# Kernel optimization log

Measured on AMD Instinct MI355X. Metric: run time of the kernel, lower is better.

## Reference

```python
import jax, jax.numpy as jnp
import numpy as np
from jax import lax

BATCH, C, HH, WW = 4, 3, 512, 512


def _dark_min(x, patch):
    # min over channels, reflect-pad, min over patch x patch window (torch unfold+min)
    pad = (patch - 1) // 2
    m = jnp.min(x, axis=1, keepdims=True)                      # [B,1,H,W]
    m = jnp.pad(m, ((0, 0), (0, 0), (pad, pad), (pad, pad)), mode='reflect')
    return lax.reduce_window(m, jnp.array(jnp.inf, m.dtype), lax.min,
                             (1, 1, patch, patch), (1, 1, 1, 1), 'VALID')


def _soft_thresh(x, lam):
    return jnp.sign(x) * jnp.maximum(jnp.abs(x) - lam, 0.0)


def _conv3x3(x, w):
    return lax.conv_general_dilated(x, w, (1, 1), 'SAME',
                                    dimension_numbers=('NCHW', 'OIHW', 'NCHW'))


def setup_inputs() -> dict:
    key = jax.random.key(0)
    names = ['I', 't_p', 'B_p', 'B', 't', 'J', 'G', 'H', 'P', 'Q', 'u', 'v', 'X', 'Y']
    keys = jax.random.split(key, len(names) + 2)
    inp = {n: jax.random.uniform(keys[i], (BATCH, C, HH, WW), dtype=jnp.float32)
           for i, n in enumerate(names)}
    for g in ['gamma_1', 'gamma_2', 'gamma_3', 'gamma_4', 'gamma_5']:
        inp[g] = jnp.array([3.001], dtype=jnp.float32)
    inp['t1d_w'] = jax.random.normal(keys[-2], (1, 3, 1, 1), dtype=jnp.float32) * 0.3
    inp['hnet_w'] = jax.random.normal(keys[-1], (3, 3, 3, 3), dtype=jnp.float32) * 0.1
    inp['patch_size'] = 35
    return inp


def _forward(I, t_p, B_p, B, t, J, G, H, P, Q, u, v, X, Y,
             gamma_1, gamma_2, gamma_3, gamma_4, gamma_5, t1d_w, hnet_w, patch_size):
    lam1, lam2, lam3, lam4, lam5 = 1.0, 0.7, 0.3, 1.0, 1.0

    # ---- get_mean_value + mapping_index (vectorized over batch) ----
    mean = jnp.mean(J, axis=(2, 3))                 # [B,3]
    idx = jnp.argsort(mean, axis=1)                 # ascending, like torch.sort
    ms = jnp.take_along_axis(mean, idx, axis=1)     # sorted means
    gather = lambda k: jnp.take_along_axis(J, idx[:, k][:, None, None, None], axis=1)
    J_l, J_m, J_s = gather(2), gather(1), gather(0)           # [B,1,H,W]
    bar = lambda k: ms[:, k][:, None, None, None]
    J_m = J_m + (bar(2) - bar(1)) * J_l
    J_s = J_s + (bar(2) - bar(0)) * J_l
    ch = jnp.arange(3)[None, :]                     # scatter channels back
    J = jnp.where((ch == idx[:, 1:2])[:, :, None, None], J_m, J)
    J = jnp.where((ch == idx[:, 0:1])[:, :, None, None], J_s, J)

    # ---- B update (spatial mean broadcast back) ----
    Bn = (lam3 * B_p - lam1 * (J * t - I) * (1.0 - t)) / (lam1 * (1.0 - t) ** 2 + lam3)
    Bn = jnp.mean(Bn, axis=(2, 3), keepdims=True) * jnp.ones_like(I)

    # ---- t update + 1x1 conv + channel replicate ----
    tn = (lam2 * t_p + gamma_4 * H - lam1 * (Bn - I) * (J - Bn) - X) / \
         (lam1 * (J - Bn) ** 2 + lam2 + gamma_4)
    t1 = jnp.einsum('oc,bchw->bohw', t1d_w[:, :, 0, 0], tn)   # [B,1,H,W]
    tn = jnp.concatenate([t1, t1, t1], axis=1)

    # ---- J, u, v updates ----
    Jn = (lam1 * (tn * (I - Bn * (1.0 - tn))) + gamma_3 * G + gamma_4 * u
          - gamma_5 * v - Y + gamma_5) / (lam1 * tn * tn + gamma_3 + gamma_4 + gamma_5)
    un = (gamma_1 * u + gamma_4 * Jn) / (gamma_1 + gamma_4)
    vn = (gamma_2 * v - gamma_5 * Jn + gamma_5) / (gamma_2 + gamma_5)

    # ---- H_Net (conv stand-in for RDN), dual updates ----
    Hn = _conv3x3(tn + X / gamma_4, hnet_w)
    Xn = X + gamma_4 * (tn - Hn)
    Yn = Y + gamma_3 * (Jn - G)

    # ---- dark channel + soft threshold ----
    M_u = _dark_min(un, patch_size)
    M_v = _dark_min(vn, patch_size)
    Pn = _soft_thresh(M_u, lam4 / gamma_1)
    Qn = _soft_thresh(M_v, lam5 / gamma_1)

    return (Bn, tn, Jn, G, Hn, Pn, Qn, un, vn, Xn, Yn, gamma_3)


def reference(I, t_p, B_p, B, t, J, G, H, P, Q, u, v, X, Y,
              gamma_1, gamma_2, gamma_3, gamma_4, gamma_5, t1d_w, hnet_w, patch_size):
    return _forward(I, t_p, B_p, B, t, J, G, H, P, Q, u, v, X, Y,
                    gamma_1, gamma_2, gamma_3, gamma_4, gamma_5, t1d_w, hnet_w, patch_size)
```

## Files before the change

kernel.cpp:

```cpp
#include <hip/hip_runtime.h>
#include <math.h>

#define W_ 512
#define H_ 512
#define HW_ 262144
#define HW4_ 65536
#define CHW_ 786432

#define O_Bn 0
#define O_tn 3145728
#define O_Jn 6291456
#define O_G  9437184
#define O_Hn 12582912
#define O_Pn 15728640
#define O_Qn 16777216
#define O_un 17825792
#define O_vn 20971520
#define O_Xn 24117248
#define O_Yn 27262976
#define O_g3 30408704

#define LAM2 0.7f
#define LAM3 0.3f

#define WS_SUMS   0
#define WS_ALPHA  8192
#define WS_IDX2   8204
#define WS_BNS    8208
#define WS_SCR    16384

typedef float nfloat4 __attribute__((ext_vector_type(4)));

__device__ __forceinline__ void nt_store4(float4 v, float4* p) {
    nfloat4 nv; nv.x = v.x; nv.y = v.y; nv.z = v.z; nv.w = v.w;
    __builtin_nontemporal_store(nv, (nfloat4*)p);
}

__global__ __launch_bounds__(256) void kRed(const float* __restrict__ J,
                                            const float* __restrict__ tt,
                                            const float* __restrict__ B_p,
                                            const float* __restrict__ I,
                                            float* __restrict__ sums) {
    int blk = blockIdx.x;
    int b = blk >> 7, chunk = blk & 127;
    size_t pb = (size_t)b * (CHW_ / 4);
    size_t cb = (size_t)chunk * 512;
    const float4* J4 = (const float4*)J;
    const float4* t4 = (const float4*)tt;
    const float4* B4 = (const float4*)B_p;
    const float4* I4 = (const float4*)I;

    float aJ[3] = {0.f, 0.f, 0.f};
    float a1[3] = {0.f, 0.f, 0.f};
    float a2[9] = {0.f, 0.f, 0.f, 0.f, 0.f, 0.f, 0.f, 0.f, 0.f};

    #pragma unroll
    for (int k = 0; k < 2; ++k) {
        size_t o = cb + threadIdx.x + k * 256;
        float4 j0 = J4[pb + 0 * HW4_ + o];
        float4 j1 = J4[pb + 1 * HW4_ + o];
        float4 j2 = J4[pb + 2 * HW4_ + o];
        #pragma unroll
        for (int c = 0; c < 3; ++c) {
            float4 tv = t4[pb + (size_t)c * HW4_ + o];
            float4 bp = B4[pb + (size_t)c * HW4_ + o];
            float4 iv = I4[pb + (size_t)c * HW4_ + o];
            float4 jc = (c == 0) ? j0 : (c == 1 ? j1 : j2);
#define REDC(m) { \
            float omt = 1.f - tv.m; \
            float r = 1.f / (omt * omt + LAM3); \
            float g = tv.m * omt * r; \
            aJ[c] += jc.m; \
            a1[c] += (LAM3 * bp.m - (jc.m * tv.m - iv.m) * omt) * r; \
            a2[0 * 3 + c] += j0.m * g; \
            a2[1 * 3 + c] += j1.m * g; \
            a2[2 * 3 + c] += j2.m * g; }
            REDC(x) REDC(y) REDC(z) REDC(w)
#undef REDC
        }
    }

    float vals[15];
    #pragma unroll
    for (int c = 0; c < 3; ++c) { vals[c] = aJ[c]; vals[3 + c] = a1[c]; }
    #pragma unroll
    for (int s = 0; s < 9; ++s) vals[6 + s] = a2[s];

    __shared__ float lds[4][15];
    int lane = threadIdx.x & 63, w = threadIdx.x >> 6;
    #pragma unroll
    for (int s = 0; s < 15; ++s) {
        float v = vals[s];
        #pragma unroll
        for (int off = 32; off; off >>= 1) v += __shfl_down(v, off, 64);
        if (lane == 0) lds[w][s] = v;
    }
    __syncthreads();
    if (threadIdx.x < 15) {
        int s = threadIdx.x;
        sums[blk * 16 + s] = lds[0][s] + lds[1][s] + lds[2][s] + lds[3][s];
    }
}

__global__ __launch_bounds__(256) void kFin(const float* __restrict__ sums,
                     float* __restrict__ alpha, int* __restrict__ idx2,
                     float* __restrict__ BnS,
                     const float* __restrict__ g3p, float* __restrict__ outg3) {
    __shared__ float part[64][4];
    __shared__ float tot[4][15];
    int t = threadIdx.x;
    int g = t >> 2, sub = t & 3;
    if (g < 60) {
        int b = g / 15, s = g % 15;
        const float* p = sums + (size_t)b * 128 * 16 + s;
        float acc = 0.f;
        #pragma unroll 8
        for (int ch = sub; ch < 128; ch += 4) acc += p[ch * 16];
        part[g][sub] = acc;
    }
    __syncthreads();
    if (t < 60) {
        tot[t / 15][t % 15] = (part[t][0] + part[t][1]) + (part[t][2] + part[t][3]);
    }
    __syncthreads();
    if (t < 4) {
        const float invHW = 1.0f / (float)HW_;
        float m[3] = {tot[t][0] * invHW, tot[t][1] * invHW, tot[t][2] * invHW};
        int r[3];
        #pragma unroll
        for (int i = 0; i < 3; ++i) {
            int ri = 0;
            #pragma unroll
            for (int j = 0; j < 3; ++j)
                if (j != i && (m[j] < m[i] || (m[j] == m[i] && j < i))) ri++;
            r[i] = ri;
        }
        int idx[3]; float ms[3];
        #pragma unroll
        for (int i = 0; i < 3; ++i) { idx[r[i]] = i; ms[r[i]] = m[i]; }
        idx2[t] = idx[2];
        float a[3] = {0.f, 0.f, 0.f};
        a[idx[1]] = ms[2] - ms[1];
        a[idx[0]] = ms[2] - ms[0];
        #pragma unroll
        for (int c = 0; c < 3; ++c) {
            alpha[t * 3 + c] = a[c];
            BnS[t * 3 + c] = (tot[t][3 + c] - a[c] * tot[t][6 + idx[2] * 3 + c]) * invHW;
        }
    }
    if (t == 0) *outg3 = g3p[0];
}

__global__ __launch_bounds__(256) void kMain(
    const float* __restrict__ I, const float* __restrict__ t_p,
    const float* __restrict__ Hm, const float* __restrict__ Xm,
    const float* __restrict__ J, const float* __restrict__ u,
    const float* __restrict__ v, const float* __restrict__ Y,
    const float* __restrict__ G,
    const float* __restrict__ g1p, const float* __restrict__ g2p,
    const float* __restrict__ g3p, const float* __restrict__ g4p,
    const float* __restrict__ g5p, const float* __restrict__ t1w,
    const float* __restrict__ alpha, const int* __restrict__ idx2,
    const float* __restrict__ BnS,
    float* __restrict__ out, float* __restrict__ scr)
{
    __shared__ float pad[2][2][560];

    int id = blockIdx.x * 256 + threadIdx.x;
    int b = id >> 16, q = id & (HW4_ - 1);
    float g1 = g1p[0], g2 = g2p[0], g3 = g3p[0], g4 = g4p[0], g5 = g5p[0];
    float wc[3] = {t1w[0], t1w[1], t1w[2]};
    int i2 = idx2[b];
    size_t pb = (size_t)b * (CHW_ / 4);
    const float4* I4p = (const float4*)I;
    const float4* tp4p = (const float4*)t_p;
    const float4* H4p = (const float4*)Hm;
    const float4* X4p = (const float4*)Xm;
    const float4* J4p = (const float4*)J;
    const float4* u4p = (const float4*)u;
    const float4* v4p = (const float4*)v;
    const float4* Y4p = (const float4*)Y;
    const float4* G4p = (const float4*)G;
    float4* o4 = (float4*)out;

    float4 Jl = J4p[pb + (size_t)i2 * HW4_ + q];
    float4 t1 = make_float4(0.f, 0.f, 0.f, 0.f);
    float4 Isv[3]; float Bsv[3];
    const float den2 = LAM2 + g4;
    #pragma unroll
    for (int c = 0; c < 3; ++c) {
        size_t o = pb + (size_t)c * HW4_ + q;
        float4 I4 = I4p[o], tp4 = tp4p[o], H4 = H4p[o], X4 = X4p[o], Jv = J4p[o];
        float al = alpha[b * 3 + c], Bnv = BnS[b * 3 + c];
        float wcc = wc[c];
#define STEP1(m) { \
        float d_ = (Jv.m + al * Jl.m) - Bnv; \
        float tnr_ = (LAM2 * tp4.m + g4 * H4.m - (Bnv - I4.m) * d_ - X4.m) / (d_ * d_ + den2); \
        t1.m += wcc * tnr_; }
        STEP1(x) STEP1(y) STEP1(z) STEP1(w)
#undef STEP1
        Isv[c] = I4; Bsv[c] = Bnv;
    }
    float g345 = g3 + g4 + g5;
    float4 invDen;
    invDen.x = 1.f / (t1.x * t1.x + g345);
    invDen.y = 1.f / (t1.y * t1.y + g345);
    invDen.z = 1.f / (t1.z * t1.z + g345);
    invDen.w = 1.f / (t1.w * t1.w + g345);
    float invDu = 1.f / (g1 + g4), invDv = 1.f / (g2 + g5);
    float4 cu = make_float4(1e30f, 1e30f, 1e30f, 1e30f);
    float4 cv = cu;
    #pragma unroll
    for (int c = 0; c < 3; ++c) {
        size_t o = pb + (size_t)c * HW4_ + q;
        float4 u4 = u4p[o], v4 = v4p[o], Y4 = Y4p[o], G4 = G4p[o];
        float Bnv = Bsv[c];
        float4 Jn4, un4, vn4, Yn4;
#define STEP2(m) { \
        float Jn_ = (t1.m * (Isv[c].m - Bnv * (1.f - t1.m)) + g3 * G4.m + g4 * u4.m \
                     - g5 * v4.m - Y4.m + g5) * invDen.m; \
        float un_ = (g1 * u4.m + g4 * Jn_) * invDu; \
        float vn_ = (g2 * v4.m - g5 * Jn_ + g5) * invDv; \
        Jn4.m = Jn_; un4.m = un_; vn4.m = vn_; \
        Yn4.m = Y4.m + g3 * (Jn_ - G4.m); \
        cu.m = fminf(cu.m, un_); cv.m = fminf(cv.m, vn_); }
        STEP2(x) STEP2(y) STEP2(z) STEP2(w)
#undef STEP2
        nt_store4(make_float4(Bnv, Bnv, Bnv, Bnv), &o4[O_Bn / 4 + o]);
        o4[O_tn / 4 + o] = t1;
        nt_store4(Jn4, &o4[O_Jn / 4 + o]);
        nt_store4(G4,  &o4[O_G  / 4 + o]);
        nt_store4(un4, &o4[O_un / 4 + o]);
        nt_store4(vn4, &o4[O_vn / 4 + o]);
        nt_store4(Yn4, &o4[O_Yn / 4 + o]);
    }

    int t = threadIdx.x;
    int rrow = t >> 7;
    int x0 = (t & 127) * 4;
    pad[0][rrow][17 + x0 + 0] = cu.x;
    pad[0][rrow][17 + x0 + 1] = cu.y;
    pad[0][rrow][17 + x0 + 2] = cu.z;
    pad[0][rrow][17 + x0 + 3] = cu.w;
    pad[1][rrow][17 + x0 + 0] = cv.x;
    pad[1][rrow][17 + x0 + 1] = cv.y;
    pad[1][rrow][17 + x0 + 2] = cv.z;
    pad[1][rrow][17 + x0 + 3] = cv.w;
    __syncthreads();
    if (t < 136) {
        int which = t / 34, e = t % 34;
        int tens = which >> 1, rw = which & 1;
        int j   = (e < 17) ? e : (529 + (e - 17));
        int src = (e < 17) ? (34 - j) : (1056 - j);
        pad[tens][rw][j] = pad[tens][rw][src];
    }
    __syncthreads();

    int y0b = (blockIdx.x & 255) * 2;
    int yg = y0b + rrow;
    #pragma unroll
    for (int tens = 0; tens < 2; ++tens) {
        const float* rowp = &pad[tens][rrow][0];
        const float4* rp4 = (const float4*)(rowp + x0);
        float4 qv = rp4[0];
        float a0 = qv.x, a1 = qv.y, a2 = qv.z;
        float mc = qv.w;
        #pragma unroll
        for (int i = 1; i < 8; ++i) {
            qv = rp4[i];
            mc = fminf(mc, fminf(fminf(qv.x, qv.y), fminf(qv.z, qv.w)));
        }
        qv = rp4[8];
        mc = fminf(mc, fminf(qv.x, fminf(qv.y, qv.z)));
        float a35 = qv.w;
        qv = rp4[9];
        float a36 = qv.x, a37 = qv.y;
        float4 r;
        r.x = fminf(fminf(a0, a1), fminf(a2, mc));
        r.y = fminf(fminf(a1, a2), fminf(mc, a35));
        r.z = fminf(fminf(a2, mc), fminf(a35, a36));
        r.w = fminf(fminf(mc, a35), fminf(a36, a37));
        *(float4*)(scr + (size_t)(tens * 4 + b) * HW_ + yg * W_ + x0) = r;
    }
}

__global__ __launch_bounds__(256) void kTail(const float* __restrict__ scr,
                                             const float* __restrict__ hw,
                                             const float* __restrict__ g1p,
                                             const float* __restrict__ g4p,
                                             float* __restrict__ out) {
    __shared__ float A_lds[3][4][528];
    __shared__ float wsh[81];
    int t = threadIdx.x;

    if (blockIdx.x < 2048) {
        int tensor = blockIdx.x >> 10;
        int lid = ((blockIdx.x & 1023) << 8) + t;
        int b = lid >> 16, qq = lid & (HW4_ - 1);
        int y = qq >> 7, xq = (qq & 127) << 2;
        const float* R = scr + (size_t)(tensor * 4 + b) * HW_;
        float4 m = make_float4(1e30f, 1e30f, 1e30f, 1e30f);
        #pragma unroll
        for (int k = 0; k < 35; ++k) {
            int yy = y + k - 17;
            yy = yy < 0 ? -yy : (yy >= H_ ? 2 * H_ - 2 - yy : yy);
            float4 r4 = *(const float4*)(R + yy * W_ + xq);
            m.x = fminf(m.x, r4.x); m.y = fminf(m.y, r4.y);
            m.z = fminf(m.z, r4.z); m.w = fminf(m.w, r4.w);
        }
        float lam = 1.0f / g1p[0];
        float4 r;
#define SOFT(m_, r_) { float s = (m_ > 0.f) ? 1.f : (m_ < 0.f ? -1.f : 0.f); \
                       r_ = s * fmaxf(fabsf(m_) - lam, 0.f); }
        SOFT(m.x, r.x) SOFT(m.y, r.y) SOFT(m.z, r.z) SOFT(m.w, r.w)
#undef SOFT
        nt_store4(r, (float4*)(out + (tensor ? O_Qn : O_Pn) + b * HW_ + y * W_ + xq));
    } else {
        int cblk = blockIdx.x - 2048;
        int b = cblk >> 8;
        int y0 = (cblk & 255) * 2;
        float g4 = g4p[0], ig4 = 1.f / g4;
        const float* tn0 = out + O_tn + (size_t)b * CHW_;
        const float* Xb  = out + O_Xn;
        (void)Xb;
        if (t < 81) wsh[t] = hw[t];
        #pragma unroll
        for (int k = 0; k < 6; ++k) {
            int g = t + 256 * k;
            int i = g >> 9, r = (g >> 7) & 3, xq = (g & 127) << 2;
            int yy = y0 - 1 + r;
            float4 A4;
            if (yy >= 0 && yy < H_) {
                const float* Xrow =  nullptr;
                (void)Xrow;
                A4 = make_float4(0.f, 0.f, 0.f, 0.f);
            }
            (void)A4; (void)i; (void)r; (void)xq; (void)yy;
        }
    }
}

__global__ __launch_bounds__(256) void kTail2(const float* __restrict__ scr,
                                              const float* __restrict__ Xm,
                                              const float* __restrict__ hw,
                                              const float* __restrict__ g1p,
                                              const float* __restrict__ g4p,
                                              float* __restrict__ out) {
    __shared__ float A_lds[3][4][528];
    __shared__ float wsh[81];
    int t = threadIdx.x;

    if (blockIdx.x < 2048) {
        int tensor = blockIdx.x >> 10;
        int lid = ((blockIdx.x & 1023) << 8) + t;
        int b = lid >> 16, qq = lid & (HW4_ - 1);
        int y = qq >> 7, xq = (qq & 127) << 2;
        const float* R = scr + (size_t)(tensor * 4 + b) * HW_;
        float4 m = make_float4(1e30f, 1e30f, 1e30f, 1e30f);
        #pragma unroll
        for (int k = 0; k < 35; ++k) {
            int yy = y + k - 17;
            yy = yy < 0 ? -yy : (yy >= H_ ? 2 * H_ - 2 - yy : yy);
            float4 r4 = *(const float4*)(R + yy * W_ + xq);
            m.x = fminf(m.x, r4.x); m.y = fminf(m.y, r4.y);
            m.z = fminf(m.z, r4.z); m.w = fminf(m.w, r4.w);
        }
        float lam = 1.0f / g1p[0];
        float4 r;
#define SOFT(m_, r_) { float s = (m_ > 0.f) ? 1.f : (m_ < 0.f ? -1.f : 0.f); \
                       r_ = s * fmaxf(fabsf(m_) - lam, 0.f); }
        SOFT(m.x, r.x) SOFT(m.y, r.y) SOFT(m.z, r.z) SOFT(m.w, r.w)
#undef SOFT
        nt_store4(r, (float4*)(out + (tensor ? O_Qn : O_Pn) + b * HW_ + y * W_ + xq));
    } else {
        int cblk = blockIdx.x - 2048;
        int b = cblk >> 8;
        int y0 = (cblk & 255) * 2;
        float g4 = g4p[0], ig4 = 1.f / g4;
        const float* tn0 = out + O_tn + (size_t)b * CHW_;
        if (t < 81) wsh[t] = hw[t];
        #pragma unroll
        for (int k = 0; k < 6; ++k) {
            int g = t + 256 * k;
            int i = g >> 9, r = (g >> 7) & 3, xq = (g & 127) << 2;
            int yy = y0 - 1 + r;
            float4 A4 = make_float4(0.f, 0.f, 0.f, 0.f);
            if (yy >= 0 && yy < H_) {
                float4 tn4 = *(const float4*)(tn0 + yy * W_ + xq);
                float4 X4  = *(const float4*)(Xm + (size_t)(b * 3 + i) * HW_ + yy * W_ + xq);
                A4.x = tn4.x + X4.x * ig4; A4.y = tn4.y + X4.y * ig4;
                A4.z = tn4.z + X4.z * ig4; A4.w = tn4.w + X4.w * ig4;
            }
            *(float4*)(&A_lds[i][r][4 + xq]) = A4;
        }
        if (t < 24) {
            int pair = t >> 1, side = t & 1;
            A_lds[pair >> 2][pair & 3][side ? 516 : 3] = 0.f;
        }
        __syncthreads();

        int tl = t & 127, r_out = t >> 7;
        float acc[3][4] = {{0.f,0.f,0.f,0.f},{0.f,0.f,0.f,0.f},{0.f,0.f,0.f,0.f}};
        #pragma unroll
        for (int i = 0; i < 3; ++i) {
            #pragma unroll
            for (int ky = 0; ky < 3; ++ky) {
                const float* Ar = &A_lds[i][r_out + ky][0];
                const float* wp0 = &wsh[0 * 27 + i * 9 + ky * 3];
                const float* wp1 = &wsh[1 * 27 + i * 9 + ky * 3];
                const float* wp2 = &wsh[2 * 27 + i * 9 + ky * 3];
                float w00 = wp0[0], w01 = wp0[1], w02 = wp0[2];
                float w10 = wp1[0], w11 = wp1[1], w12 = wp1[2];
                float w20 = wp2[0], w21 = wp2[1], w22 = wp2[2];
                #pragma unroll
                for (int j = 0; j < 4; ++j) {
                    int x = tl + 128 * j;
                    float am = Ar[3 + x], a0 = Ar[4 + x], ap = Ar[5 + x];
                    acc[0][j] += w00 * am + w01 * a0 + w02 * ap;
                    acc[1][j] += w10 * am + w11 * a0 + w12 * ap;
                    acc[2][j] += w20 * am + w21 * a0 + w22 * ap;
                }
            }
        }
        int yg = y0 + r_out;
        #pragma unroll
        for (int o = 0; o < 3; ++o) {
            #pragma unroll
            for (int j = 0; j < 4; ++j) {
                int x = tl + 128 * j;
                size_t oo = (size_t)(b * 3 + o) * HW_ + yg * W_ + x;
                float hn = acc[o][j];
                float Ac = A_lds[o][r_out + 1][4 + x];
                __builtin_nontemporal_store(hn, &out[O_Hn + oo]);
                __builtin_nontemporal_store(g4 * (Ac - hn), &out[O_Xn + oo]);
            }
        }
    }
}

extern "C" void kernel_launch(void* const* d_in, const int* in_sizes, int n_in,
                              void* d_out, int out_size, void* d_ws, size_t ws_size,
                              hipStream_t stream) {
    (void)in_sizes; (void)n_in; (void)out_size; (void)ws_size;
    const float* I   = (const float*)d_in[0];
    const float* t_p = (const float*)d_in[1];
    const float* B_p = (const float*)d_in[2];
    const float* tt  = (const float*)d_in[4];
    const float* J   = (const float*)d_in[5];
    const float* G   = (const float*)d_in[6];
    const float* Hm  = (const float*)d_in[7];
    const float* u   = (const float*)d_in[10];
    const float* v   = (const float*)d_in[11];
    const float* X   = (const float*)d_in[12];
    const float* Y   = (const float*)d_in[13];
    const float* g1  = (const float*)d_in[14];
    const float* g2  = (const float*)d_in[15];
    const float* g3  = (const float*)d_in[16];
    const float* g4  = (const float*)d_in[17];
    const float* g5  = (const float*)d_in[18];
    const float* t1w = (const float*)d_in[19];
    const float* hw  = (const float*)d_in[20];
    float* out = (float*)d_out;
    float* ws  = (float*)d_ws;

    float* sums  = ws + WS_SUMS;
    float* alpha = ws + WS_ALPHA;
    int*   idx2  = (int*)(ws + WS_IDX2);
    float* BnS   = ws + WS_BNS;
    float* scr   = ws + WS_SCR;

    kRed<<<512, 256, 0, stream>>>(J, tt, B_p, I, sums);
    kFin<<<1, 256, 0, stream>>>(sums, alpha, idx2, BnS, g3, out + O_g3);
    kMain<<<1024, 256, 0, stream>>>(I, t_p, Hm, X, J, u, v, Y, G,
                                    g1, g2, g3, g4, g5, t1w, alpha, idx2, BnS,
                                    out, scr);
    kTail2<<<3072, 256, 0, stream>>>(scr, X, hw, g1, g4, out);
}
```

Before: 310.6 us.

## Fuse conv stage into main kernel and replace finalize kernel with atomics

The single-block finalize kernel is removed: kRed now atomically accumulates per-batch sums into a zeroed workspace, and each kMain block recomputes sort/alpha/BnS from those sums in one thread. The 3x3 conv (Hn, Xn) moves into kMain, which builds its LDS input tile from registers plus recomputed halo rows, so tn is no longer re-read from global memory. The tail kernel keeps only the vertical min and soft threshold. The cost is recomputing t1 for halo rows, a memset launch, atomic order nondeterminism, and more LDS and registers in kMain.

```diff
diff --git a/kernel.cpp b/kernel.cpp
--- a/kernel.cpp
+++ b/kernel.cpp
@@ -23,10 +23,7 @@
 #define LAM2 0.7f
 #define LAM3 0.3f
 
-#define WS_SUMS   0
-#define WS_ALPHA  8192
-#define WS_IDX2   8204
-#define WS_BNS    8208
+#define WS_ACC    0
 #define WS_SCR    16384
 
 typedef float nfloat4 __attribute__((ext_vector_type(4)));
@@ -40,7 +37,7 @@
                                             const float* __restrict__ tt,
                                             const float* __restrict__ B_p,
                                             const float* __restrict__ I,
-                                            float* __restrict__ sums) {
+                                            float* __restrict__ acc) {
     int blk = blockIdx.x;
     int b = blk >> 7, chunk = blk & 127;
     size_t pb = (size_t)b * (CHW_ / 4);
@@ -98,57 +95,9 @@
     __syncthreads();
     if (threadIdx.x < 15) {
         int s = threadIdx.x;
-        sums[blk * 16 + s] = lds[0][s] + lds[1][s] + lds[2][s] + lds[3][s];
-    }
-}
-
-__global__ __launch_bounds__(256) void kFin(const float* __restrict__ sums,
-                     float* __restrict__ alpha, int* __restrict__ idx2,
-                     float* __restrict__ BnS,
-                     const float* __restrict__ g3p, float* __restrict__ outg3) {
-    __shared__ float part[64][4];
-    __shared__ float tot[4][15];
-    int t = threadIdx.x;
-    int g = t >> 2, sub = t & 3;
-    if (g < 60) {
-        int b = g / 15, s = g % 15;
-        const float* p = sums + (size_t)b * 128 * 16 + s;
-        float acc = 0.f;
-        #pragma unroll 8
-        for (int ch = sub; ch < 128; ch += 4) acc += p[ch * 16];
-        part[g][sub] = acc;
-    }
-    __syncthreads();
-    if (t < 60) {
-        tot[t / 15][t % 15] = (part[t][0] + part[t][1]) + (part[t][2] + part[t][3]);
-    }
-    __syncthreads();
-    if (t < 4) {
-        const float invHW = 1.0f / (float)HW_;
-        float m[3] = {tot[t][0] * invHW, tot[t][1] * invHW, tot[t][2] * invHW};
-        int r[3];
-        #pragma unroll
-        for (int i = 0; i < 3; ++i) {
-            int ri = 0;
-            #pragma unroll
-            for (int j = 0; j < 3; ++j)
-                if (j != i && (m[j] < m[i] || (m[j] == m[i] && j < i))) ri++;
-            r[i] = ri;
-        }
-        int idx[3]; float ms[3];
-        #pragma unroll
-        for (int i = 0; i < 3; ++i) { idx[r[i]] = i; ms[r[i]] = m[i]; }
-        idx2[t] = idx[2];
-        float a[3] = {0.f, 0.f, 0.f};
-        a[idx[1]] = ms[2] - ms[1];
-        a[idx[0]] = ms[2] - ms[0];
-        #pragma unroll
-        for (int c = 0; c < 3; ++c) {
-            alpha[t * 3 + c] = a[c];
-            BnS[t * 3 + c] = (tot[t][3 + c] - a[c] * tot[t][6 + idx[2] * 3 + c]) * invHW;
-        }
-    }
-    if (t == 0) *outg3 = g3p[0];
+        atomicAdd(&acc[b * 15 + s],
+                  (lds[0][s] + lds[1][s]) + (lds[2][s] + lds[3][s]));
+    }
 }
 
 __global__ __launch_bounds__(256) void kMain(
@@ -160,18 +109,60 @@
     const float* __restrict__ g1p, const float* __restrict__ g2p,
     const float* __restrict__ g3p, const float* __restrict__ g4p,
     const float* __restrict__ g5p, const float* __restrict__ t1w,
-    const float* __restrict__ alpha, const int* __restrict__ idx2,
-    const float* __restrict__ BnS,
+    const float* __restrict__ hw, const float* __restrict__ acc,
     float* __restrict__ out, float* __restrict__ scr)
 {
     __shared__ float pad[2][2][560];
-
-    int id = blockIdx.x * 256 + threadIdx.x;
-    int b = id >> 16, q = id & (HW4_ - 1);
+    __shared__ float A_lds[3][4][528];
+    __shared__ float wsh[81];
+    __shared__ float sAlpha[3], sBnS[3];
+    __shared__ int sI2;
+
+    int t = threadIdx.x;
+    int b = blockIdx.x >> 8;
+    int y0b = (blockIdx.x & 255) * 2;
     float g1 = g1p[0], g2 = g2p[0], g3 = g3p[0], g4 = g4p[0], g5 = g5p[0];
+    float ig4 = 1.f / g4;
+
+    if (t == 0) {
+        const float invHW = 1.0f / (float)HW_;
+        float tot[15];
+        #pragma unroll
+        for (int s = 0; s < 15; ++s) tot[s] = acc[b * 15 + s];
+        float m[3] = {tot[0] * invHW, tot[1] * invHW, tot[2] * invHW};
+        int r[3];
+        #pragma unroll
+        for (int i = 0; i < 3; ++i) {
+            int ri = 0;
+            #pragma unroll
+            for (int j = 0; j < 3; ++j)
+                if (j != i && (m[j] < m[i] || (m[j] == m[i] && j < i))) ri++;
+            r[i] = ri;
+        }
+        int idx[3]; float ms[3];
+        #pragma unroll
+        for (int i = 0; i < 3; ++i) { idx[r[i]] = i; ms[r[i]] = m[i]; }
+        sI2 = idx[2];
+        float a[3] = {0.f, 0.f, 0.f};
+        a[idx[1]] = ms[2] - ms[1];
+        a[idx[0]] = ms[2] - ms[0];
+        #pragma unroll
+        for (int c = 0; c < 3; ++c) {
+            sAlpha[c] = a[c];
+            sBnS[c] = (tot[3 + c] - a[c] * tot[6 + idx[2] * 3 + c]) * invHW;
+        }
+        if (blockIdx.x == 0) out[O_g3] = g3;
+    }
+    if (t < 81) wsh[t] = hw[t];
+    __syncthreads();
+
+    int rrow = t >> 7;
+    int xq = t & 127;
+    int x0 = xq * 4;
+    size_t pb = (size_t)b * (CHW_ / 4);
+    size_t q = (size_t)(y0b + rrow) * 128 + xq;
     float wc[3] = {t1w[0], t1w[1], t1w[2]};
-    int i2 = idx2[b];
-    size_t pb = (size_t)b * (CHW_ / 4);
+    int i2 = sI2;
     const float4* I4p = (const float4*)I;
     const float4* tp4p = (const float4*)t_p;
     const float4* H4p = (const float4*)Hm;
@@ -185,13 +176,13 @@
 
     float4 Jl = J4p[pb + (size_t)i2 * HW4_ + q];
     float4 t1 = make_float4(0.f, 0.f, 0.f, 0.f);
-    float4 Isv[3]; float Bsv[3];
+    float4 Isv[3], Xsv[3]; float Bsv[3];
     const float den2 = LAM2 + g4;
     #pragma unroll
     for (int c = 0; c < 3; ++c) {
         size_t o = pb + (size_t)c * HW4_ + q;
         float4 I4 = I4p[o], tp4 = tp4p[o], H4 = H4p[o], X4 = X4p[o], Jv = J4p[o];
-        float al = alpha[b * 3 + c], Bnv = BnS[b * 3 + c];
+        float al = sAlpha[c], Bnv = sBnS[c];
         float wcc = wc[c];
 #define STEP1(m) { \
         float d_ = (Jv.m + al * Jl.m) - Bnv; \
@@ -199,7 +190,7 @@
         t1.m += wcc * tnr_; }
         STEP1(x) STEP1(y) STEP1(z) STEP1(w)
 #undef STEP1
-        Isv[c] = I4; Bsv[c] = Bnv;
+        Isv[c] = I4; Xsv[c] = X4; Bsv[c] = Bnv;
     }
     float g345 = g3 + g4 + g5;
     float4 invDen;
@@ -227,17 +218,17 @@
         STEP2(x) STEP2(y) STEP2(z) STEP2(w)
 #undef STEP2
         nt_store4(make_float4(Bnv, Bnv, Bnv, Bnv), &o4[O_Bn / 4 + o]);
-        o4[O_tn / 4 + o] = t1;
+        nt_store4(t1,  &o4[O_tn / 4 + o]);
         nt_store4(Jn4, &o4[O_Jn / 4 + o]);
         nt_store4(G4,  &o4[O_G  / 4 + o]);
         nt_store4(un4, &o4[O_un / 4 + o]);
         nt_store4(vn4, &o4[O_vn / 4 + o]);
         nt_store4(Yn4, &o4[O_Yn / 4 + o]);
-    }
-
-    int t = threadIdx.x;
-    int rrow = t >> 7;
-    int x0 = (t & 127) * 4;
+        float4 A4;
+        A4.x = t1.x + Xsv[c].x * ig4; A4.y = t1.y + Xsv[c].y * ig4;
+        A4.z = t1.z + Xsv[c].z * ig4; A4.w = t1.w + Xsv[c].w * ig4;
+        *(float4*)(&A_lds[c][1 + rrow][4 + x0]) = A4;
+    }
     pad[0][rrow][17 + x0 + 0] = cu.x;
     pad[0][rrow][17 + x0 + 1] = cu.y;
     pad[0][rrow][17 + x0 + 2] = cu.z;
@@ -246,7 +237,49 @@
     pad[1][rrow][17 + x0 + 1] = cv.y;
     pad[1][rrow][17 + x0 + 2] = cv.z;
     pad[1][rrow][17 + x0 + 3] = cv.w;
+
+    {
+        int hr = (rrow == 0) ? (y0b - 1) : (y0b + 2);
+        int ar = (rrow == 0) ? 0 : 3;
+        if (hr >= 0 && hr < H_) {
+            size_t hq = (size_t)hr * 128 + xq;
+            float4 Jlh = J4p[pb + (size_t)i2 * HW4_ + hq];
+            float4 t1h = make_float4(0.f, 0.f, 0.f, 0.f);
+            float4 Xh[3];
+            #pragma unroll
+            for (int c = 0; c < 3; ++c) {
+                size_t o = pb + (size_t)c * HW4_ + hq;
+                float4 I4 = I4p[o], tp4 = tp4p[o], H4 = H4p[o], X4 = X4p[o], Jv = J4p[o];
+                float al = sAlpha[c], Bnv = sBnS[c];
+                float wcc = wc[c];
+#define STEP1H(m) { \
+                float d_ = (Jv.m + al * Jlh.m) - Bnv; \
+                float tnr_ = (LAM2 * tp4.m + g4 * H4.m - (Bnv - I4.m) * d_ - X4.m) / (d_ * d_ + den2); \
+                t1h.m += wcc * tnr_; }
+                STEP1H(x) STEP1H(y) STEP1H(z) STEP1H(w)
+#undef STEP1H
+                Xh[c] = X4;
+            }
+            #pragma unroll
+            for (int c = 0; c < 3; ++c) {
+                float4 A4;
+                A4.x = t1h.x + Xh[c].x * ig4; A4.y = t1h.y + Xh[c].y * ig4;
+                A4.z = t1h.z + Xh[c].z * ig4; A4.w = t1h.w + Xh[c].w * ig4;
+                *(float4*)(&A_lds[c][ar][4 + x0]) = A4;
+            }
+        } else {
+            float4 z = make_float4(0.f, 0.f, 0.f, 0.f);
+            #pragma unroll
+            for (int c = 0; c < 3; ++c)
+                *(float4*)(&A_lds[c][ar][4 + x0]) = z;
+        }
+    }
+    if (t < 24) {
+        int pair = t >> 1, side = t & 1;
+        A_lds[pair >> 2][pair & 3][side ? 516 : 3] = 0.f;
+    }
     __syncthreads();
+
     if (t < 136) {
         int which = t / 34, e = t % 34;
         int tens = which >> 1, rw = which & 1;
@@ -256,7 +289,6 @@
     }
     __syncthreads();
 
-    int y0b = (blockIdx.x & 255) * 2;
     int yg = y0b + rrow;
     #pragma unroll
     for (int tens = 0; tens < 2; ++tens) {
@@ -282,125 +314,10 @@
         r.w = fminf(fminf(mc, a35), fminf(a36, a37));
         *(float4*)(scr + (size_t)(tens * 4 + b) * HW_ + yg * W_ + x0) = r;
     }
-}
-
-__global__ __launch_bounds__(256) void kTail(const float* __restrict__ scr,
-                                             const float* __restrict__ hw,
-                                             const float* __restrict__ g1p,
-                                             const float* __restrict__ g4p,
-                                             float* __restrict__ out) {
-    __shared__ float A_lds[3][4][528];
-    __shared__ float wsh[81];
-    int t = threadIdx.x;
-
-    if (blockIdx.x < 2048) {
-        int tensor = blockIdx.x >> 10;
-        int lid = ((blockIdx.x & 1023) << 8) + t;
-        int b = lid >> 16, qq = lid & (HW4_ - 1);
-        int y = qq >> 7, xq = (qq & 127) << 2;
-        const float* R = scr + (size_t)(tensor * 4 + b) * HW_;
-        float4 m = make_float4(1e30f, 1e30f, 1e30f, 1e30f);
-        #pragma unroll
-        for (int k = 0; k < 35; ++k) {
-            int yy = y + k - 17;
-            yy = yy < 0 ? -yy : (yy >= H_ ? 2 * H_ - 2 - yy : yy);
-            float4 r4 = *(const float4*)(R + yy * W_ + xq);
-            m.x = fminf(m.x, r4.x); m.y = fminf(m.y, r4.y);
-            m.z = fminf(m.z, r4.z); m.w = fminf(m.w, r4.w);
-        }
-        float lam = 1.0f / g1p[0];
-        float4 r;
-#define SOFT(m_, r_) { float s = (m_ > 0.f) ? 1.f : (m_ < 0.f ? -1.f : 0.f); \
-                       r_ = s * fmaxf(fabsf(m_) - lam, 0.f); }
-        SOFT(m.x, r.x) SOFT(m.y, r.y) SOFT(m.z, r.z) SOFT(m.w, r.w)
-#undef SOFT
-        nt_store4(r, (float4*)(out + (tensor ? O_Qn : O_Pn) + b * HW_ + y * W_ + xq));
-    } else {
-        int cblk = blockIdx.x - 2048;
-        int b = cblk >> 8;
-        int y0 = (cblk & 255) * 2;
-        float g4 = g4p[0], ig4 = 1.f / g4;
-        const float* tn0 = out + O_tn + (size_t)b * CHW_;
-        const float* Xb  = out + O_Xn;
-        (void)Xb;
-        if (t < 81) wsh[t] = hw[t];
-        #pragma unroll
-        for (int k = 0; k < 6; ++k) {
-            int g = t + 256 * k;
-            int i = g >> 9, r = (g >> 7) & 3, xq = (g & 127) << 2;
-            int yy = y0 - 1 + r;
-            float4 A4;
-            if (yy >= 0 && yy < H_) {
-                const float* Xrow =  nullptr;
-                (void)Xrow;
-                A4 = make_float4(0.f, 0.f, 0.f, 0.f);
-            }
-            (void)A4; (void)i; (void)r; (void)xq; (void)yy;
-        }
-    }
-}
-
-__global__ __launch_bounds__(256) void kTail2(const float* __restrict__ scr,
-                                              const float* __restrict__ Xm,
-                                              const float* __restrict__ hw,
-                                              const float* __restrict__ g1p,
-                                              const float* __restrict__ g4p,
-                                              float* __restrict__ out) {
-    __shared__ float A_lds[3][4][528];
-    __shared__ float wsh[81];
-    int t = threadIdx.x;
-
-    if (blockIdx.x < 2048) {
-        int tensor = blockIdx.x >> 10;
-        int lid = ((blockIdx.x & 1023) << 8) + t;
-        int b = lid >> 16, qq = lid & (HW4_ - 1);
-        int y = qq >> 7, xq = (qq & 127) << 2;
-        const float* R = scr + (size_t)(tensor * 4 + b) * HW_;
-        float4 m = make_float4(1e30f, 1e30f, 1e30f, 1e30f);
-        #pragma unroll
-        for (int k = 0; k < 35; ++k) {
-            int yy = y + k - 17;
-            yy = yy < 0 ? -yy : (yy >= H_ ? 2 * H_ - 2 - yy : yy);
-            float4 r4 = *(const float4*)(R + yy * W_ + xq);
-            m.x = fminf(m.x, r4.x); m.y = fminf(m.y, r4.y);
-            m.z = fminf(m.z, r4.z); m.w = fminf(m.w, r4.w);
-        }
-        float lam = 1.0f / g1p[0];
-        float4 r;
-#define SOFT(m_, r_) { float s = (m_ > 0.f) ? 1.f : (m_ < 0.f ? -1.f : 0.f); \
-                       r_ = s * fmaxf(fabsf(m_) - lam, 0.f); }
-        SOFT(m.x, r.x) SOFT(m.y, r.y) SOFT(m.z, r.z) SOFT(m.w, r.w)
-#undef SOFT
-        nt_store4(r, (float4*)(out + (tensor ? O_Qn : O_Pn) + b * HW_ + y * W_ + xq));
-    } else {
-        int cblk = blockIdx.x - 2048;
-        int b = cblk >> 8;
-        int y0 = (cblk & 255) * 2;
-        float g4 = g4p[0], ig4 = 1.f / g4;
-        const float* tn0 = out + O_tn + (size_t)b * CHW_;
-        if (t < 81) wsh[t] = hw[t];
-        #pragma unroll
-        for (int k = 0; k < 6; ++k) {
-            int g = t + 256 * k;
-            int i = g >> 9, r = (g >> 7) & 3, xq = (g & 127) << 2;
-            int yy = y0 - 1 + r;
-            float4 A4 = make_float4(0.f, 0.f, 0.f, 0.f);
-            if (yy >= 0 && yy < H_) {
-                float4 tn4 = *(const float4*)(tn0 + yy * W_ + xq);
-                float4 X4  = *(const float4*)(Xm + (size_t)(b * 3 + i) * HW_ + yy * W_ + xq);
-                A4.x = tn4.x + X4.x * ig4; A4.y = tn4.y + X4.y * ig4;
-                A4.z = tn4.z + X4.z * ig4; A4.w = tn4.w + X4.w * ig4;
-            }
-            *(float4*)(&A_lds[i][r][4 + xq]) = A4;
-        }
-        if (t < 24) {
-            int pair = t >> 1, side = t & 1;
-            A_lds[pair >> 2][pair & 3][side ? 516 : 3] = 0.f;
-        }
-        __syncthreads();
-
+
+    {
         int tl = t & 127, r_out = t >> 7;
-        float acc[3][4] = {{0.f,0.f,0.f,0.f},{0.f,0.f,0.f,0.f},{0.f,0.f,0.f,0.f}};
+        float cacc[3][4] = {{0.f,0.f,0.f,0.f},{0.f,0.f,0.f,0.f},{0.f,0.f,0.f,0.f}};
         #pragma unroll
         for (int i = 0; i < 3; ++i) {
             #pragma unroll
@@ -416,26 +333,53 @@
                 for (int j = 0; j < 4; ++j) {
                     int x = tl + 128 * j;
                     float am = Ar[3 + x], a0 = Ar[4 + x], ap = Ar[5 + x];
-                    acc[0][j] += w00 * am + w01 * a0 + w02 * ap;
-                    acc[1][j] += w10 * am + w11 * a0 + w12 * ap;
-                    acc[2][j] += w20 * am + w21 * a0 + w22 * ap;
+                    cacc[0][j] += w00 * am + w01 * a0 + w02 * ap;
+                    cacc[1][j] += w10 * am + w11 * a0 + w12 * ap;
+                    cacc[2][j] += w20 * am + w21 * a0 + w22 * ap;
                 }
             }
         }
-        int yg = y0 + r_out;
+        int ygc = y0b + r_out;
         #pragma unroll
         for (int o = 0; o < 3; ++o) {
             #pragma unroll
             for (int j = 0; j < 4; ++j) {
                 int x = tl + 128 * j;
-                size_t oo = (size_t)(b * 3 + o) * HW_ + yg * W_ + x;
-                float hn = acc[o][j];
+                size_t oo = (size_t)(b * 3 + o) * HW_ + (size_t)ygc * W_ + x;
+                float hn = cacc[o][j];
                 float Ac = A_lds[o][r_out + 1][4 + x];
                 __builtin_nontemporal_store(hn, &out[O_Hn + oo]);
                 __builtin_nontemporal_store(g4 * (Ac - hn), &out[O_Xn + oo]);
             }
         }
     }
+}
+
+__global__ __launch_bounds__(256) void kVMin(const float* __restrict__ scr,
+                                             const float* __restrict__ g1p,
+                                             float* __restrict__ out) {
+    int t = threadIdx.x;
+    int tensor = blockIdx.x >> 10;
+    int lid = ((blockIdx.x & 1023) << 8) + t;
+    int b = lid >> 16, qq = lid & (HW4_ - 1);
+    int y = qq >> 7, xq = (qq & 127) << 2;
+    const float* R = scr + (size_t)(tensor * 4 + b) * HW_;
+    float4 m = make_float4(1e30f, 1e30f, 1e30f, 1e30f);
+    #pragma unroll
+    for (int k = 0; k < 35; ++k) {
+        int yy = y + k - 17;
+        yy = yy < 0 ? -yy : (yy >= H_ ? 2 * H_ - 2 - yy : yy);
+        float4 r4 = *(const float4*)(R + yy * W_ + xq);
+        m.x = fminf(m.x, r4.x); m.y = fminf(m.y, r4.y);
+        m.z = fminf(m.z, r4.z); m.w = fminf(m.w, r4.w);
+    }
+    float lam = 1.0f / g1p[0];
+    float4 r;
+#define SOFT(m_, r_) { float s = (m_ > 0.f) ? 1.f : (m_ < 0.f ? -1.f : 0.f); \
+                       r_ = s * fmaxf(fabsf(m_) - lam, 0.f); }
+    SOFT(m.x, r.x) SOFT(m.y, r.y) SOFT(m.z, r.z) SOFT(m.w, r.w)
+#undef SOFT
+    nt_store4(r, (float4*)(out + (tensor ? O_Qn : O_Pn) + b * HW_ + y * W_ + xq));
 }
 
 extern "C" void kernel_launch(void* const* d_in, const int* in_sizes, int n_in,
@@ -463,16 +407,12 @@
     float* out = (float*)d_out;
     float* ws  = (float*)d_ws;
 
-    float* sums  = ws + WS_SUMS;
-    float* alpha = ws + WS_ALPHA;
-    int*   idx2  = (int*)(ws + WS_IDX2);
-    float* BnS   = ws + WS_BNS;
-    float* scr   = ws + WS_SCR;
-
-    kRed<<<512, 256, 0, stream>>>(J, tt, B_p, I, sums);
-    kFin<<<1, 256, 0, stream>>>(sums, alpha, idx2, BnS, g3, out + O_g3);
+    float* acc = ws + WS_ACC;
+    float* scr = ws + WS_SCR;
+
+    hipMemsetAsync(acc, 0, 64 * sizeof(float), stream);
+    kRed<<<512, 256, 0, stream>>>(J, tt, B_p, I, acc);
     kMain<<<1024, 256, 0, stream>>>(I, t_p, Hm, X, J, u, v, Y, G,
-                                    g1, g2, g3, g4, g5, t1w, alpha, idx2, BnS,
-                                    out, scr);
-    kTail2<<<3072, 256, 0, stream>>>(scr, X, hw, g1, g4, out);
+                                    g1, g2, g3, g4, g5, t1w, hw, acc, out, scr);
+    kVMin<<<2048, 256, 0, stream>>>(scr, g1, out);
 }
```

After: 308.7 us. Within noise of the previous version (-0.6%).
